# Kernel tuning notes

Measured on AMD Instinct MI355X. Metric: run time of the kernel, lower is better.

The kernel has to match this reference:

```python
import jax, jax.numpy as jnp
import numpy as np

N_NODES = 100000
DROPOUT_P = 0.2


def _gcn_conv(x, W, b, src, dst, n_nodes):
    # PyG GCNConv: h = x @ W; add self-loops; sym-norm deg^-1/2 aggregation; + bias
    h = x @ W  # [N, D_out]
    loops = jnp.arange(n_nodes, dtype=src.dtype)
    src_all = jnp.concatenate([src, loops])
    dst_all = jnp.concatenate([dst, loops])
    deg = jax.ops.segment_sum(jnp.ones_like(dst_all, dtype=h.dtype), dst_all,
                              num_segments=n_nodes)  # includes self-loops
    dinv = jnp.where(deg > 0, jax.lax.rsqrt(deg), 0.0)
    norm = dinv[src_all] * dinv[dst_all]  # [E+N]
    msg = h[src_all] * norm[:, None]      # gather + scale
    out = jax.ops.segment_sum(msg, dst_all, num_segments=n_nodes)  # scatter-add
    return out + b


def setup_inputs() -> dict:
    key = jax.random.key(0)
    k1, k2, k3, k4 = jax.random.split(key, 4)
    x = jax.random.normal(k1, (N_NODES, 128), dtype=jnp.float32)
    edge_index = jax.random.randint(k2, (2, 1600000), 0, N_NODES, dtype=jnp.int64)
    W1 = jax.random.normal(k3, (128, 64), dtype=jnp.float32) * (1.0 / np.sqrt(128))
    b1 = jnp.zeros((64,), dtype=jnp.float32)
    W2 = jax.random.normal(k4, (64, 32), dtype=jnp.float32) * (1.0 / np.sqrt(64))
    b2 = jnp.zeros((32,), dtype=jnp.float32)
    return {"x": x, "edge_index": edge_index, "W1": W1, "b1": b1, "W2": W2, "b2": b2}


def reference(x, edge_index, W1, b1, W2, b2):
    src, dst = edge_index[0], edge_index[1]
    h1 = _gcn_conv(x, W1, b1, src, dst, N_NODES)
    h1 = jax.nn.relu(h1)
    # F.dropout defaults to training=True -> apply inverted dropout with fixed key
    keep = jax.random.bernoulli(jax.random.key(42), 1.0 - DROPOUT_P, h1.shape)
    h1 = jnp.where(keep, h1 / (1.0 - DROPOUT_P), 0.0)
    h2 = _gcn_conv(h1, W2, b2, src, dst, N_NODES)
    return h2
```

## Files before the change

kernel.cpp:

```cpp
#include <hip/hip_runtime.h>
#include <stdint.h>

#define DIN 128
#define D1 64
#define D2 32
#define MAXDEG 48
#define BCAP 4608
#define CBLK 8192

__device__ __forceinline__ unsigned short f2bf(float v) {
  unsigned u = __float_as_uint(v);
  unsigned r = u + 0x7fffu + ((u >> 16) & 1u);
  return (unsigned short)(r >> 16);
}
__device__ __forceinline__ float bflo(unsigned u) { return __uint_as_float(u << 16); }
__device__ __forceinline__ float bfhi(unsigned u) { return __uint_as_float(u & 0xffff0000u); }

__device__ __forceinline__ unsigned rotl32(unsigned x, int r) {
  return (x << r) | (x >> (32 - r));
}

__device__ __forceinline__ unsigned threefry_fold(unsigned ctr) {
  unsigned k0 = 0u, k1 = 42u;
  unsigned ks0 = k0, ks1 = k1, ks2 = k0 ^ k1 ^ 0x1BD11BDAu;
  unsigned x0 = 0u, x1 = ctr;
  x0 += ks0; x1 += ks1;
#define TF_ROUND(r) { x0 += x1; x1 = rotl32(x1, (r)); x1 ^= x0; }
  TF_ROUND(13) TF_ROUND(15) TF_ROUND(26) TF_ROUND(6)
  x0 += ks1; x1 += ks2 + 1u;
  TF_ROUND(17) TF_ROUND(29) TF_ROUND(16) TF_ROUND(24)
  x0 += ks2; x1 += ks0 + 2u;
  TF_ROUND(13) TF_ROUND(15) TF_ROUND(26) TF_ROUND(6)
  x0 += ks0; x1 += ks1 + 3u;
  TF_ROUND(17) TF_ROUND(29) TF_ROUND(16) TF_ROUND(24)
  x0 += ks1; x1 += ks2 + 4u;
  TF_ROUND(13) TF_ROUND(15) TF_ROUND(26) TF_ROUND(6)
  x0 += ks2; x1 += ks0 + 5u;
#undef TF_ROUND
  return x0 ^ x1;
}

__device__ __forceinline__ float dropout_scale(unsigned idx) {
  unsigned bits = threefry_fold(idx);
  float u = __uint_as_float((bits >> 9) | 0x3f800000u) - 1.0f;
  return (u < 0.8f) ? 1.25f : 0.0f;
}

__device__ __forceinline__ uint4 grow64(const unsigned short* p, int s, int fc) {
  return *(const uint4*)((const char*)p + (((unsigned)s << 7) + ((unsigned)fc << 1)));
}
__device__ __forceinline__ uint4 grow32(const unsigned short* p, int s, int fc) {
  return *(const uint4*)((const char*)p + (((unsigned)s << 6) + ((unsigned)fc << 1)));
}

__device__ __forceinline__ void addpk(float2& a, unsigned u) {
  a.x += bflo(u);
  a.y += bfhi(u);
}
__device__ __forceinline__ void addpkm(float2& a, unsigned u, float m) {
  a.x = fmaf(m, bflo(u), a.x);
  a.y = fmaf(m, bfhi(u), a.y);
}

template <int K>
__device__ __forceinline__ void gather_acc1(float2 (&acc)[4], int sv, int cnt, int d, int fc,
                                            const unsigned short* __restrict__ h1p, int eslot) {
  uint4 v[K];
#pragma unroll
  for (int seg = 0; seg < K - 1; seg++) {
    int s = __shfl(sv, seg * 8 + eslot, 64);
    v[seg] = grow64(h1p, s, fc);
  }
  const int elast = (K - 1) * 8 + eslot;
  const bool ok = elast < cnt;
  {
    int s = __shfl(sv, elast, 64);
    v[K - 1] = grow64(h1p, ok ? s : d, fc);
  }
#pragma unroll
  for (int seg = 0; seg < K - 1; seg++) {
    addpk(acc[0], v[seg].x); addpk(acc[1], v[seg].y);
    addpk(acc[2], v[seg].z); addpk(acc[3], v[seg].w);
  }
  const float m = ok ? 1.0f : 0.0f;
  addpkm(acc[0], v[K - 1].x, m); addpkm(acc[1], v[K - 1].y, m);
  addpkm(acc[2], v[K - 1].z, m); addpkm(acc[3], v[K - 1].w, m);
}

template <int K>
__device__ __forceinline__ void gather_acc2(float2 (&acc)[4], int sv, int cnt, int d, int fc,
                                            const unsigned short* __restrict__ h2p, int eslot) {
  uint4 v[K];
#pragma unroll
  for (int seg = 0; seg < K - 1; seg++) {
    int s = __shfl(sv, seg * 16 + eslot, 64);
    v[seg] = grow32(h2p, s, fc);
  }
  const int elast = (K - 1) * 16 + eslot;
  const bool ok = elast < cnt;
  {
    int s = __shfl(sv, elast, 64);
    v[K - 1] = grow32(h2p, ok ? s : d, fc);
  }
#pragma unroll
  for (int seg = 0; seg < K - 1; seg++) {
    addpk(acc[0], v[seg].x); addpk(acc[1], v[seg].y);
    addpk(acc[2], v[seg].z); addpk(acc[3], v[seg].w);
  }
  const float m = ok ? 1.0f : 0.0f;
  addpkm(acc[0], v[K - 1].x, m); addpkm(acc[1], v[K - 1].y, m);
  addpkm(acc[2], v[K - 1].z, m); addpkm(acc[3], v[K - 1].w, m);
}

__global__ __launch_bounds__(256) void bin_kernel(const int* __restrict__ src,
                                                  const int* __restrict__ dst,
                                                  int* __restrict__ cursor,
                                                  uint2* __restrict__ binned,
                                                  int E, int NBK) {
  __shared__ int cnt[512];
  __shared__ int cbase[512];
  __shared__ int dstbuf[CBLK];
  const int tid = threadIdx.x;
  const int e0 = blockIdx.x * CBLK;

  for (int b = tid; b < NBK; b += 256) cnt[b] = 0;
  __syncthreads();

#pragma unroll 4
  for (int i = 0; i < CBLK / 256; i++) {
    int e = e0 + tid + 256 * i;
    int dv = (e < E) ? dst[e] : -1;
    dstbuf[tid + 256 * i] = dv;
    if (dv >= 0) atomicAdd(&cnt[dv >> 8], 1);
  }
  __syncthreads();

  for (int b = tid; b < NBK; b += 256) {
    int c = cnt[b];
    if (c > 0) cbase[b] = b * BCAP + atomicAdd(&cursor[b], c);
    cnt[b] = 0;
  }
  __syncthreads();

#pragma unroll 4
  for (int i = 0; i < CBLK / 256; i++) {
    int e = e0 + tid + 256 * i;
    int d = dstbuf[tid + 256 * i];
    if (d >= 0) {
      int b = d >> 8;
      int rk = atomicAdd(&cnt[b], 1);
      int pos = cbase[b] + rk;
      if (pos - b * BCAP < BCAP)
        binned[pos] = make_uint2((unsigned)d, (unsigned)src[e]);
    }
  }
}

__global__ __launch_bounds__(256) void ellbuild_kernel(const uint2* __restrict__ binned,
                                                       const int* __restrict__ cursor,
                                                       int* __restrict__ deg,
                                                       float* __restrict__ dinv,
                                                       int* __restrict__ ell, int N) {
  __shared__ int r[256];
  const int tid = threadIdx.x;
  const int b = blockIdx.x;
  const int nodebase = b << 8;
  r[tid] = 0;
  __syncthreads();

  int cnt = cursor[b];
  if (cnt > BCAP) cnt = BCAP;
  const uint2* seg = binned + (size_t)b * BCAP;
  for (int i = tid; i < cnt; i += 256) {
    uint2 p = seg[i];
    int local = (int)p.x - nodebase;
    int rk = atomicAdd(&r[local], 1);
    if (rk < MAXDEG) ell[(int)p.x * MAXDEG + rk] = (int)p.y;
  }
  __syncthreads();

  int node = nodebase + tid;
  if (node < N) {
    int dg = r[tid];
    deg[node] = dg;
    dinv[node] = (float)(1.0 / sqrt((double)(dg + 1)));
  }
}

__global__ __launch_bounds__(256) void gemm1_kernel(const float* __restrict__ x,
                                                    const float* __restrict__ W1,
                                                    const float* __restrict__ dinv,
                                                    unsigned short* __restrict__ h1p, int N) {
  __shared__ float xT[32][65];
  __shared__ float Wl[32][D1];
  const int tid = threadIdx.x;
  const int rowbase = blockIdx.x * 64;
  const int tx = tid & 15;
  const int ty = tid >> 4;
  float acc[4][4];
#pragma unroll
  for (int i = 0; i < 4; i++)
#pragma unroll
    for (int j = 0; j < 4; j++) acc[i][j] = 0.f;

  for (int c4 = 0; c4 < 4; c4++) {
    const int k0 = c4 * 32;
#pragma unroll
    for (int i = 0; i < 2; i++) {
      int f = tid + 256 * i;
      int row = f >> 3;
      int kq = (f & 7) * 4;
      int gr = rowbase + row;
      float4 vv = make_float4(0.f, 0.f, 0.f, 0.f);
      if (gr < N) vv = *(const float4*)(x + (size_t)gr * DIN + k0 + kq);
      xT[kq + 0][row] = vv.x;
      xT[kq + 1][row] = vv.y;
      xT[kq + 2][row] = vv.z;
      xT[kq + 3][row] = vv.w;
    }
#pragma unroll
    for (int i = 0; i < 2; i++) {
      int f = tid + 256 * i;
      int k = f >> 4;
      int cc = (f & 15) * 4;
      *(float4*)&Wl[k][cc] = *(const float4*)(W1 + (size_t)(k0 + k) * D1 + cc);
    }
    __syncthreads();
#pragma unroll 4
    for (int k = 0; k < 32; k++) {
      float4 a = *(const float4*)&xT[k][4 * ty];
      float4 b = *(const float4*)&Wl[k][4 * tx];
      float av[4] = {a.x, a.y, a.z, a.w};
      float bv[4] = {b.x, b.y, b.z, b.w};
#pragma unroll
      for (int i = 0; i < 4; i++)
#pragma unroll
        for (int j = 0; j < 4; j++) acc[i][j] = fmaf(av[i], bv[j], acc[i][j]);
    }
    __syncthreads();
  }

#pragma unroll
  for (int i = 0; i < 4; i++) {
    int gr = rowbase + 4 * ty + i;
    if (gr < N) {
      float di = dinv[gr];
      ushort4 o;
      o.x = f2bf(acc[i][0] * di);
      o.y = f2bf(acc[i][1] * di);
      o.z = f2bf(acc[i][2] * di);
      o.w = f2bf(acc[i][3] * di);
      *(ushort4*)(h1p + (size_t)gr * D1 + 4 * tx) = o;
    }
  }
}

__global__ __launch_bounds__(256) void agg1_kernel(const int* __restrict__ deg,
                                                   const float* __restrict__ dinv,
                                                   const int* __restrict__ ell,
                                                   const unsigned short* __restrict__ h1p,
                                                   const float* __restrict__ b1,
                                                   float* __restrict__ h1d, int N) {
  __shared__ float red[4][528];
  const int wslot = __builtin_amdgcn_readfirstlane(threadIdx.x >> 6);
  const int d = blockIdx.x * 4 + wslot;
  const int lane = threadIdx.x & 63;
  const int eslot = lane >> 3;
  const int fc = (lane & 7) << 3;
  const int cnt = min(deg[d], MAXDEG);
  const int base = d * MAXDEG;
  const int f = fc + eslot;

  int sv = ell[base + lane];
  uint4 self = grow64(h1p, d, fc);
  const float di = dinv[d];
  const float bias = b1[f];
  const float drop = dropout_scale((unsigned)(d * D1 + f));

  float2 acc[4];
  {
    float m = (eslot == 0) ? 1.0f : 0.0f;
    acc[0] = make_float2(m * bflo(self.x), m * bfhi(self.x));
    acc[1] = make_float2(m * bflo(self.y), m * bfhi(self.y));
    acc[2] = make_float2(m * bflo(self.z), m * bfhi(self.z));
    acc[3] = make_float2(m * bflo(self.w), m * bfhi(self.w));
  }

  switch ((cnt + 7) >> 3) {
    case 6: gather_acc1<6>(acc, sv, cnt, d, fc, h1p, eslot); break;
    case 5: gather_acc1<5>(acc, sv, cnt, d, fc, h1p, eslot); break;
    case 4: gather_acc1<4>(acc, sv, cnt, d, fc, h1p, eslot); break;
    case 3: gather_acc1<3>(acc, sv, cnt, d, fc, h1p, eslot); break;
    case 2: gather_acc1<2>(acc, sv, cnt, d, fc, h1p, eslot); break;
    case 1: gather_acc1<1>(acc, sv, cnt, d, fc, h1p, eslot); break;
    default: break;
  }

  float* wred = red[wslot];
  *(float4*)&wred[eslot * 66 + fc]     = make_float4(acc[0].x, acc[0].y, acc[1].x, acc[1].y);
  *(float4*)&wred[eslot * 66 + fc + 4] = make_float4(acc[2].x, acc[2].y, acc[3].x, acc[3].y);
  float vsum = 0.f;
#pragma unroll
  for (int e = 0; e < 8; e++) vsum += wred[e * 66 + f];

  float o = fmaf(di, vsum, bias);
  o = fmaxf(o, 0.0f);
  o *= drop;
  h1d[(size_t)d * D1 + f] = o;
}

__global__ __launch_bounds__(256) void gemm2_kernel(const float* __restrict__ h1d,
                                                    const float* __restrict__ W2,
                                                    const float* __restrict__ dinv,
                                                    unsigned short* __restrict__ h2p, int N) {
  __shared__ float hT[D1][129];
  __shared__ float Wl[D1][D2];
  const int tid = threadIdx.x;
  const int rowbase = blockIdx.x * 128;

#pragma unroll
  for (int i = 0; i < 8; i++) {
    int f = tid + 256 * i;
    int row = f >> 4;
    int kq = (f & 15) * 4;
    int gr = rowbase + row;
    float4 v = make_float4(0.f, 0.f, 0.f, 0.f);
    if (gr < N) v = *(const float4*)(h1d + (size_t)gr * D1 + kq);
    hT[kq + 0][row] = v.x;
    hT[kq + 1][row] = v.y;
    hT[kq + 2][row] = v.z;
    hT[kq + 3][row] = v.w;
  }
#pragma unroll
  for (int i = 0; i < 2; i++) {
    int f = tid + 256 * i;
    int k = f >> 3;
    int c = (f & 7) * 4;
    *(float4*)&Wl[k][c] = *(const float4*)(W2 + (size_t)k * D2 + c);
  }
  __syncthreads();

  const int tx = tid & 7;
  const int ty = tid >> 3;
  float acc[4][4];
#pragma unroll
  for (int i = 0; i < 4; i++)
#pragma unroll
    for (int j = 0; j < 4; j++) acc[i][j] = 0.f;

#pragma unroll 4
  for (int k = 0; k < D1; k++) {
    float4 a = *(const float4*)&hT[k][4 * ty];
    float4 b = *(const float4*)&Wl[k][4 * tx];
    float av[4] = {a.x, a.y, a.z, a.w};
    float bv[4] = {b.x, b.y, b.z, b.w};
#pragma unroll
    for (int i = 0; i < 4; i++)
#pragma unroll
      for (int j = 0; j < 4; j++) acc[i][j] = fmaf(av[i], bv[j], acc[i][j]);
  }

#pragma unroll
  for (int i = 0; i < 4; i++) {
    int gr = rowbase + 4 * ty + i;
    if (gr < N) {
      float di = dinv[gr];
      ushort4 o;
      o.x = f2bf(acc[i][0] * di);
      o.y = f2bf(acc[i][1] * di);
      o.z = f2bf(acc[i][2] * di);
      o.w = f2bf(acc[i][3] * di);
      *(ushort4*)(h2p + (size_t)gr * D2 + 4 * tx) = o;
    }
  }
}

__global__ __launch_bounds__(256) void agg2_kernel(const int* __restrict__ deg,
                                                   const float* __restrict__ dinv,
                                                   const int* __restrict__ ell,
                                                   const unsigned short* __restrict__ h2p,
                                                   const float* __restrict__ b2,
                                                   float* __restrict__ out, int N) {
  __shared__ float red[4][544];
  const int wslot = __builtin_amdgcn_readfirstlane(threadIdx.x >> 6);
  const int d = blockIdx.x * 4 + wslot;
  const int lane = threadIdx.x & 63;
  const int eslot = lane >> 2;
  const int fc = (lane & 3) << 3;
  const int cnt = min(deg[d], MAXDEG);
  const int base = d * MAXDEG;

  int sv = ell[base + lane];
  uint4 self = grow32(h2p, d, fc);
  const float di = dinv[d];

  float2 acc[4];
  {
    float m = (eslot == 0) ? 1.0f : 0.0f;
    acc[0] = make_float2(m * bflo(self.x), m * bfhi(self.x));
    acc[1] = make_float2(m * bflo(self.y), m * bfhi(self.y));
    acc[2] = make_float2(m * bflo(self.z), m * bfhi(self.z));
    acc[3] = make_float2(m * bflo(self.w), m * bfhi(self.w));
  }

  switch ((cnt + 15) >> 4) {
    case 3: gather_acc2<3>(acc, sv, cnt, d, fc, h2p, eslot); break;
    case 2: gather_acc2<2>(acc, sv, cnt, d, fc, h2p, eslot); break;
    case 1: gather_acc2<1>(acc, sv, cnt, d, fc, h2p, eslot); break;
    default: break;
  }

  float* wred = red[wslot];
  *(float4*)&wred[eslot * 34 + fc]     = make_float4(acc[0].x, acc[0].y, acc[1].x, acc[1].y);
  *(float4*)&wred[eslot * 34 + fc + 4] = make_float4(acc[2].x, acc[2].y, acc[3].x, acc[3].y);
  const int f = fc + (eslot & 7);
  const int ebase = (lane >= 32) ? 8 : 0;
  float vsum = 0.f;
#pragma unroll
  for (int e = 0; e < 8; e++) vsum += wred[(ebase + e) * 34 + f];
  vsum += __shfl_down(vsum, 32, 64);

  if (lane < 32) {
    out[(size_t)d * D2 + f] = fmaf(di, vsum, b2[f]);
  }
}

extern "C" void kernel_launch(void* const* d_in, const int* in_sizes, int n_in,
                              void* d_out, int out_size, void* d_ws, size_t ws_size,
                              hipStream_t stream) {
  const float* x  = (const float*)d_in[0];
  const int*   ei = (const int*)d_in[1];
  const float* W1 = (const float*)d_in[2];
  const float* b1 = (const float*)d_in[3];
  const float* W2 = (const float*)d_in[4];
  const float* b2 = (const float*)d_in[5];
  const int N = in_sizes[0] / DIN;
  const int E = in_sizes[1] / 2;
  const int NBK = (N + 255) >> 8;
  const int* src = ei;
  const int* dst = ei + E;
  float* out = (float*)d_out;

  char* ws = (char*)d_ws;
  size_t off = 0;
  auto alloc = [&](size_t bytes) -> char* {
    char* p = ws + off;
    off += (bytes + 255) / 256 * 256;
    return p;
  };
  unsigned short* h1p = (unsigned short*)alloc((size_t)N * D1 * 2);
  float*          h1d = (float*)alloc((size_t)N * D1 * 4);
  int*            ell = (int*)alloc(((size_t)N * MAXDEG + 64) * 4);
  int*            deg = (int*)alloc((size_t)N * 4);
  float*        dinvp = (float*)alloc((size_t)N * 4);
  int*         cursor = (int*)alloc((size_t)NBK * 4);
  unsigned short* h2p = h1p;
  uint2*       binned = (uint2*)h1d;
  (void)ws_size; (void)n_in; (void)out_size;

  hipMemsetAsync(cursor, 0, (size_t)NBK * 4, stream);

  bin_kernel<<<(E + CBLK - 1) / CBLK, 256, 0, stream>>>(src, dst, cursor, binned, E, NBK);
  ellbuild_kernel<<<NBK, 256, 0, stream>>>(binned, cursor, deg, dinvp, ell, N);
  gemm1_kernel<<<(N + 63) / 64, 256, 0, stream>>>(x, W1, dinvp, h1p, N);
  agg1_kernel<<<N / 4, 256, 0, stream>>>(deg, dinvp, ell, h1p, b1, h1d, N);
  gemm2_kernel<<<(N + 127) / 128, 256, 0, stream>>>(h1d, W2, dinvp, h2p, N);
  agg2_kernel<<<N / 4, 256, 0, stream>>>(deg, dinvp, ell, h2p, b2, out, N);
}
```

Before: 245.4 us.

## Fuse edge binning with first GEMM and move source dinv scaling into aggregation

Edge binning and the first x@W1 GEMM now run as one launch, with disjoint block ranges sharing a union of shared-memory layouts, so the GEMM no longer waits on dinv and both stages can overlap. Because of that, the source-side deg^-1/2 factor is applied per edge inside agg1 through a shuffled dinv gather rather than being folded into h1. Binned entries shrink from uint2 to a single packed 32-bit word (local dst in the high byte, src in the low 24 bits), and binning switches to a block-local prefix scan with staged coalesced writes. The cost is an extra dinv gather and more multiplies in agg1, plus the assumption that node indices fit in 24 bits.

```diff
diff --git a/kernel.cpp b/kernel.cpp
--- a/kernel.cpp
+++ b/kernel.cpp
@@ -6,7 +6,8 @@
 #define D2 32
 #define MAXDEG 48
 #define BCAP 4608
-#define CBLK 8192
+#define BINBLK 4096
+#define NBKPAD 512
 
 __device__ __forceinline__ unsigned short f2bf(float v) {
   unsigned u = __float_as_uint(v);
@@ -63,28 +64,31 @@
 }
 
 template <int K>
-__device__ __forceinline__ void gather_acc1(float2 (&acc)[4], int sv, int cnt, int d, int fc,
+__device__ __forceinline__ void gather_acc1(float2 (&acc)[4], int sv, float dvv, int cnt,
+                                            int d, int fc,
                                             const unsigned short* __restrict__ h1p, int eslot) {
   uint4 v[K];
+  float dv[K];
 #pragma unroll
   for (int seg = 0; seg < K - 1; seg++) {
-    int s = __shfl(sv, seg * 8 + eslot, 64);
+    int e = seg * 8 + eslot;
+    int s = __shfl(sv, e, 64);
+    dv[seg] = __shfl(dvv, e, 64);
     v[seg] = grow64(h1p, s, fc);
   }
-  const int elast = (K - 1) * 8 + eslot;
-  const bool ok = elast < cnt;
   {
+    const int elast = (K - 1) * 8 + eslot;
+    const bool ok = elast < cnt;
     int s = __shfl(sv, elast, 64);
+    float dl = __shfl(dvv, elast, 64);
+    dv[K - 1] = ok ? dl : 0.0f;
     v[K - 1] = grow64(h1p, ok ? s : d, fc);
   }
 #pragma unroll
-  for (int seg = 0; seg < K - 1; seg++) {
-    addpk(acc[0], v[seg].x); addpk(acc[1], v[seg].y);
-    addpk(acc[2], v[seg].z); addpk(acc[3], v[seg].w);
-  }
-  const float m = ok ? 1.0f : 0.0f;
-  addpkm(acc[0], v[K - 1].x, m); addpkm(acc[1], v[K - 1].y, m);
-  addpkm(acc[2], v[K - 1].z, m); addpkm(acc[3], v[K - 1].w, m);
+  for (int seg = 0; seg < K; seg++) {
+    addpkm(acc[0], v[seg].x, dv[seg]); addpkm(acc[1], v[seg].y, dv[seg]);
+    addpkm(acc[2], v[seg].z, dv[seg]); addpkm(acc[3], v[seg].w, dv[seg]);
+  }
 }
 
 template <int K>
@@ -112,51 +116,187 @@
   addpkm(acc[2], v[K - 1].z, m); addpkm(acc[3], v[K - 1].w, m);
 }
 
-__global__ __launch_bounds__(256) void bin_kernel(const int* __restrict__ src,
-                                                  const int* __restrict__ dst,
-                                                  int* __restrict__ cursor,
-                                                  uint2* __restrict__ binned,
-                                                  int E, int NBK) {
-  __shared__ int cnt[512];
-  __shared__ int cbase[512];
-  __shared__ int dstbuf[CBLK];
+struct BinShared {
+  int cnt[NBKPAD];
+  int cnt2[NBKPAD];
+  int gdelta[NBKPAD];
+  unsigned pairbuf[BINBLK];
+};
+struct G1Shared {
+  float xT[32][65];
+  float Wl[32][D1];
+};
+union K1Shared {
+  BinShared bin;
+  G1Shared g1;
+};
+
+__global__ __launch_bounds__(256) void fused1_kernel(const int* __restrict__ src,
+                                                     const int* __restrict__ dst,
+                                                     int* __restrict__ cursor,
+                                                     unsigned* __restrict__ binned,
+                                                     int E, int NBK, int nbin,
+                                                     const float* __restrict__ x,
+                                                     const float* __restrict__ W1,
+                                                     unsigned short* __restrict__ h1p, int N) {
+  __shared__ K1Shared sh;
   const int tid = threadIdx.x;
-  const int e0 = blockIdx.x * CBLK;
-
-  for (int b = tid; b < NBK; b += 256) cnt[b] = 0;
-  __syncthreads();
-
+
+  if ((int)blockIdx.x < nbin) {
+    const int e0 = blockIdx.x * BINBLK;
+    const bool full = (e0 + BINBLK) <= E;
+
+    for (int b = tid; b < NBKPAD; b += 256) { sh.bin.cnt[b] = 0; sh.bin.cnt2[b] = 0; }
+    __syncthreads();
+
+    int dreg[16];
+    if (full) {
+#pragma unroll
+      for (int i = 0; i < 4; i++) {
+        int4 q = *(const int4*)(dst + e0 + 4 * tid + 1024 * i);
+        dreg[4 * i + 0] = q.x; dreg[4 * i + 1] = q.y;
+        dreg[4 * i + 2] = q.z; dreg[4 * i + 3] = q.w;
+      }
+    } else {
+#pragma unroll
+      for (int i = 0; i < 16; i++) {
+        int e = e0 + 4 * tid + 1024 * (i >> 2) + (i & 3);
+        dreg[i] = (e < E) ? dst[e] : -1;
+      }
+    }
+#pragma unroll
+    for (int i = 0; i < 16; i++)
+      if (dreg[i] >= 0) atomicAdd(&sh.bin.cnt[dreg[i] >> 8], 1);
+    __syncthreads();
+
+    int c0 = sh.bin.cnt[tid], c1 = sh.bin.cnt[tid + 256];
+    for (int off = 1; off < NBKPAD; off <<= 1) {
+      int a0 = sh.bin.cnt[tid];
+      int a1 = sh.bin.cnt[tid + 256];
+      int b0 = (tid >= off) ? sh.bin.cnt[tid - off] : 0;
+      int b1 = (tid + 256 >= off) ? sh.bin.cnt[tid + 256 - off] : 0;
+      __syncthreads();
+      sh.bin.cnt[tid] = a0 + b0;
+      sh.bin.cnt[tid + 256] = a1 + b1;
+      __syncthreads();
+    }
+    int lb0 = sh.bin.cnt[tid] - c0;
+    int lb1 = sh.bin.cnt[tid + 256] - c1;
+    if (tid < NBK && c0 > 0) {
+      int g = tid * BCAP + atomicAdd(&cursor[tid], c0);
+      sh.bin.gdelta[tid] = g - lb0;
+    }
+    if (tid + 256 < NBK && c1 > 0) {
+      int g = (tid + 256) * BCAP + atomicAdd(&cursor[tid + 256], c1);
+      sh.bin.gdelta[tid + 256] = g - lb1;
+    }
+    __syncthreads();
+    sh.bin.cnt[tid] = lb0;
+    sh.bin.cnt[tid + 256] = lb1;
+    __syncthreads();
+
+    int sreg[16];
+    if (full) {
+#pragma unroll
+      for (int i = 0; i < 4; i++) {
+        int4 q = *(const int4*)(src + e0 + 4 * tid + 1024 * i);
+        sreg[4 * i + 0] = q.x; sreg[4 * i + 1] = q.y;
+        sreg[4 * i + 2] = q.z; sreg[4 * i + 3] = q.w;
+      }
+    } else {
+#pragma unroll
+      for (int i = 0; i < 16; i++) {
+        int e = e0 + 4 * tid + 1024 * (i >> 2) + (i & 3);
+        sreg[i] = (e < E) ? src[e] : 0;
+      }
+    }
+#pragma unroll
+    for (int i = 0; i < 16; i++) {
+      int d = dreg[i];
+      if (d >= 0) {
+        int b = d >> 8;
+        int r = atomicAdd(&sh.bin.cnt2[b], 1);
+        sh.bin.pairbuf[sh.bin.cnt[b] + r] =
+            ((unsigned)(d & 255) << 24) | (unsigned)sreg[i];
+      }
+    }
+    __syncthreads();
+
+    const int lane = tid & 63;
+    const int wv = tid >> 6;
+    for (int b = wv; b < NBK; b += 4) {
+      int lb = sh.bin.cnt[b];
+      int c = sh.bin.cnt2[b];
+      int gd = (c > 0) ? sh.bin.gdelta[b] : 0;
+      for (int i = lane; i < c; i += 64) {
+        int gpos = gd + lb + i;
+        if (gpos - b * BCAP < BCAP)
+          binned[gpos] = sh.bin.pairbuf[lb + i];
+      }
+    }
+  } else {
+    const int rowbase = ((int)blockIdx.x - nbin) * 64;
+    const int tx = tid & 15;
+    const int ty = tid >> 4;
+    float acc[4][4];
+#pragma unroll
+    for (int i = 0; i < 4; i++)
+#pragma unroll
+      for (int j = 0; j < 4; j++) acc[i][j] = 0.f;
+
+    for (int c4 = 0; c4 < 4; c4++) {
+      const int k0 = c4 * 32;
+#pragma unroll
+      for (int i = 0; i < 2; i++) {
+        int f = tid + 256 * i;
+        int row = f >> 3;
+        int kq = (f & 7) * 4;
+        int gr = rowbase + row;
+        float4 vv = make_float4(0.f, 0.f, 0.f, 0.f);
+        if (gr < N) vv = *(const float4*)(x + (size_t)gr * DIN + k0 + kq);
+        sh.g1.xT[kq + 0][row] = vv.x;
+        sh.g1.xT[kq + 1][row] = vv.y;
+        sh.g1.xT[kq + 2][row] = vv.z;
+        sh.g1.xT[kq + 3][row] = vv.w;
+      }
+#pragma unroll
+      for (int i = 0; i < 2; i++) {
+        int f = tid + 256 * i;
+        int k = f >> 4;
+        int cc = (f & 15) * 4;
+        *(float4*)&sh.g1.Wl[k][cc] = *(const float4*)(W1 + (size_t)(k0 + k) * D1 + cc);
+      }
+      __syncthreads();
 #pragma unroll 4
-  for (int i = 0; i < CBLK / 256; i++) {
-    int e = e0 + tid + 256 * i;
-    int dv = (e < E) ? dst[e] : -1;
-    dstbuf[tid + 256 * i] = dv;
-    if (dv >= 0) atomicAdd(&cnt[dv >> 8], 1);
-  }
-  __syncthreads();
-
-  for (int b = tid; b < NBK; b += 256) {
-    int c = cnt[b];
-    if (c > 0) cbase[b] = b * BCAP + atomicAdd(&cursor[b], c);
-    cnt[b] = 0;
-  }
-  __syncthreads();
-
-#pragma unroll 4
-  for (int i = 0; i < CBLK / 256; i++) {
-    int e = e0 + tid + 256 * i;
-    int d = dstbuf[tid + 256 * i];
-    if (d >= 0) {
-      int b = d >> 8;
-      int rk = atomicAdd(&cnt[b], 1);
-      int pos = cbase[b] + rk;
-      if (pos - b * BCAP < BCAP)
-        binned[pos] = make_uint2((unsigned)d, (unsigned)src[e]);
-    }
-  }
-}
-
-__global__ __launch_bounds__(256) void ellbuild_kernel(const uint2* __restrict__ binned,
+      for (int k = 0; k < 32; k++) {
+        float4 a = *(const float4*)&sh.g1.xT[k][4 * ty];
+        float4 b = *(const float4*)&sh.g1.Wl[k][4 * tx];
+        float av[4] = {a.x, a.y, a.z, a.w};
+        float bv[4] = {b.x, b.y, b.z, b.w};
+#pragma unroll
+        for (int i = 0; i < 4; i++)
+#pragma unroll
+          for (int j = 0; j < 4; j++) acc[i][j] = fmaf(av[i], bv[j], acc[i][j]);
+      }
+      __syncthreads();
+    }
+
+#pragma unroll
+    for (int i = 0; i < 4; i++) {
+      int gr = rowbase + 4 * ty + i;
+      if (gr < N) {
+        ushort4 o;
+        o.x = f2bf(acc[i][0]);
+        o.y = f2bf(acc[i][1]);
+        o.z = f2bf(acc[i][2]);
+        o.w = f2bf(acc[i][3]);
+        *(ushort4*)(h1p + (size_t)gr * D1 + 4 * tx) = o;
+      }
+    }
+  }
+}
+
+__global__ __launch_bounds__(256) void ellbuild_kernel(const unsigned* __restrict__ binned,
                                                        const int* __restrict__ cursor,
                                                        int* __restrict__ deg,
                                                        float* __restrict__ dinv,
@@ -170,12 +310,12 @@
 
   int cnt = cursor[b];
   if (cnt > BCAP) cnt = BCAP;
-  const uint2* seg = binned + (size_t)b * BCAP;
+  const unsigned* seg = binned + (size_t)b * BCAP;
   for (int i = tid; i < cnt; i += 256) {
-    uint2 p = seg[i];
-    int local = (int)p.x - nodebase;
+    unsigned p = seg[i];
+    int local = (int)(p >> 24);
     int rk = atomicAdd(&r[local], 1);
-    if (rk < MAXDEG) ell[(int)p.x * MAXDEG + rk] = (int)p.y;
+    if (rk < MAXDEG) ell[(nodebase + local) * MAXDEG + rk] = (int)(p & 0x00FFFFFFu);
   }
   __syncthreads();
 
@@ -184,74 +324,6 @@
     int dg = r[tid];
     deg[node] = dg;
     dinv[node] = (float)(1.0 / sqrt((double)(dg + 1)));
-  }
-}
-
-__global__ __launch_bounds__(256) void gemm1_kernel(const float* __restrict__ x,
-                                                    const float* __restrict__ W1,
-                                                    const float* __restrict__ dinv,
-                                                    unsigned short* __restrict__ h1p, int N) {
-  __shared__ float xT[32][65];
-  __shared__ float Wl[32][D1];
-  const int tid = threadIdx.x;
-  const int rowbase = blockIdx.x * 64;
-  const int tx = tid & 15;
-  const int ty = tid >> 4;
-  float acc[4][4];
-#pragma unroll
-  for (int i = 0; i < 4; i++)
-#pragma unroll
-    for (int j = 0; j < 4; j++) acc[i][j] = 0.f;
-
-  for (int c4 = 0; c4 < 4; c4++) {
-    const int k0 = c4 * 32;
-#pragma unroll
-    for (int i = 0; i < 2; i++) {
-      int f = tid + 256 * i;
-      int row = f >> 3;
-      int kq = (f & 7) * 4;
-      int gr = rowbase + row;
-      float4 vv = make_float4(0.f, 0.f, 0.f, 0.f);
-      if (gr < N) vv = *(const float4*)(x + (size_t)gr * DIN + k0 + kq);
-      xT[kq + 0][row] = vv.x;
-      xT[kq + 1][row] = vv.y;
-      xT[kq + 2][row] = vv.z;
-      xT[kq + 3][row] = vv.w;
-    }
-#pragma unroll
-    for (int i = 0; i < 2; i++) {
-      int f = tid + 256 * i;
-      int k = f >> 4;
-      int cc = (f & 15) * 4;
-      *(float4*)&Wl[k][cc] = *(const float4*)(W1 + (size_t)(k0 + k) * D1 + cc);
-    }
-    __syncthreads();
-#pragma unroll 4
-    for (int k = 0; k < 32; k++) {
-      float4 a = *(const float4*)&xT[k][4 * ty];
-      float4 b = *(const float4*)&Wl[k][4 * tx];
-      float av[4] = {a.x, a.y, a.z, a.w};
-      float bv[4] = {b.x, b.y, b.z, b.w};
-#pragma unroll
-      for (int i = 0; i < 4; i++)
-#pragma unroll
-        for (int j = 0; j < 4; j++) acc[i][j] = fmaf(av[i], bv[j], acc[i][j]);
-    }
-    __syncthreads();
-  }
-
-#pragma unroll
-  for (int i = 0; i < 4; i++) {
-    int gr = rowbase + 4 * ty + i;
-    if (gr < N) {
-      float di = dinv[gr];
-      ushort4 o;
-      o.x = f2bf(acc[i][0] * di);
-      o.y = f2bf(acc[i][1] * di);
-      o.z = f2bf(acc[i][2] * di);
-      o.w = f2bf(acc[i][3] * di);
-      *(ushort4*)(h1p + (size_t)gr * D1 + 4 * tx) = o;
-    }
   }
 }
 
@@ -272,6 +344,8 @@
   const int f = fc + eslot;
 
   int sv = ell[base + lane];
+  sv = (lane < cnt) ? sv : d;
+  float dvv = dinv[sv];
   uint4 self = grow64(h1p, d, fc);
   const float di = dinv[d];
   const float bias = b1[f];
@@ -279,7 +353,7 @@
 
   float2 acc[4];
   {
-    float m = (eslot == 0) ? 1.0f : 0.0f;
+    float m = (eslot == 0) ? di : 0.0f;
     acc[0] = make_float2(m * bflo(self.x), m * bfhi(self.x));
     acc[1] = make_float2(m * bflo(self.y), m * bfhi(self.y));
     acc[2] = make_float2(m * bflo(self.z), m * bfhi(self.z));
@@ -287,12 +361,12 @@
   }
 
   switch ((cnt + 7) >> 3) {
-    case 6: gather_acc1<6>(acc, sv, cnt, d, fc, h1p, eslot); break;
-    case 5: gather_acc1<5>(acc, sv, cnt, d, fc, h1p, eslot); break;
-    case 4: gather_acc1<4>(acc, sv, cnt, d, fc, h1p, eslot); break;
-    case 3: gather_acc1<3>(acc, sv, cnt, d, fc, h1p, eslot); break;
-    case 2: gather_acc1<2>(acc, sv, cnt, d, fc, h1p, eslot); break;
-    case 1: gather_acc1<1>(acc, sv, cnt, d, fc, h1p, eslot); break;
+    case 6: gather_acc1<6>(acc, sv, dvv, cnt, d, fc, h1p, eslot); break;
+    case 5: gather_acc1<5>(acc, sv, dvv, cnt, d, fc, h1p, eslot); break;
+    case 4: gather_acc1<4>(acc, sv, dvv, cnt, d, fc, h1p, eslot); break;
+    case 3: gather_acc1<3>(acc, sv, dvv, cnt, d, fc, h1p, eslot); break;
+    case 2: gather_acc1<2>(acc, sv, dvv, cnt, d, fc, h1p, eslot); break;
+    case 1: gather_acc1<1>(acc, sv, dvv, cnt, d, fc, h1p, eslot); break;
     default: break;
   }
 
@@ -455,14 +529,16 @@
   float*        dinvp = (float*)alloc((size_t)N * 4);
   int*         cursor = (int*)alloc((size_t)NBK * 4);
   unsigned short* h2p = h1p;
-  uint2*       binned = (uint2*)h1d;
+  unsigned*    binned = (unsigned*)h1d;
   (void)ws_size; (void)n_in; (void)out_size;
 
   hipMemsetAsync(cursor, 0, (size_t)NBK * 4, stream);
 
-  bin_kernel<<<(E + CBLK - 1) / CBLK, 256, 0, stream>>>(src, dst, cursor, binned, E, NBK);
+  const int NB_BIN = (E + BINBLK - 1) / BINBLK;
+  const int NB_G1 = (N + 63) / 64;
+  fused1_kernel<<<NB_BIN + NB_G1, 256, 0, stream>>>(src, dst, cursor, binned, E, NBK, NB_BIN,
+                                                    x, W1, h1p, N);
   ellbuild_kernel<<<NBK, 256, 0, stream>>>(binned, cursor, deg, dinvp, ell, N);
-  gemm1_kernel<<<(N + 63) / 64, 256, 0, stream>>>(x, W1, dinvp, h1p, N);
   agg1_kernel<<<N / 4, 256, 0, stream>>>(deg, dinvp, ell, h1p, b1, h1d, N);
   gemm2_kernel<<<(N + 127) / 128, 256, 0, stream>>>(h1d, W2, dinvp, h2p, N);
   agg2_kernel<<<N / 4, 256, 0, stream>>>(deg, dinvp, ell, h2p, b2, out, N);
```

Measured after the change: 246.8 us. About the same (+0.6%).
